# Optimization experiments

Hardware: AMD Instinct MI355X
Metric: run time of the kernel (lower is better)

Reference implementation:

```python
import jax, jax.numpy as jnp
import numpy as np

TOPK = 10
HID = 512
RHID = 150
CH = 32


def _gru(x, Wi, Wh, bi, bh):
    """torch nn.GRU (1 layer, batch_first) with gate order r,z,n. x: [B,T,D]."""
    H = Wh.shape[1]
    xi = x @ Wi.T + bi  # [B,T,3H] precompute input projections

    def step(h, xt):
        gh = h @ Wh.T + bh
        r = jax.nn.sigmoid(xt[:, :H] + gh[:, :H])
        z = jax.nn.sigmoid(xt[:, H:2 * H] + gh[:, H:2 * H])
        n = jnp.tanh(xt[:, 2 * H:] + r * gh[:, 2 * H:])
        h_new = (1.0 - z) * n + z * h
        return h_new, h_new

    h0 = jnp.zeros((x.shape[0], H), x.dtype)
    hT, ys = jax.lax.scan(step, h0, jnp.swapaxes(xi, 0, 1))
    return jnp.swapaxes(ys, 0, 1), hT


def reference(window, emb, w_init, w_root, arma_b, Wi1, Wh1, bi1, bh1,
              Wi2, Wh2, bi2, bh2, W_fc, b_fc):
    B, T, N = window.shape
    # --- SingleEmbedding (post-warmup): cosine similarity + per-row top-k ---
    Wn = emb / jnp.clip(jnp.linalg.norm(emb, axis=1, keepdims=True), 1e-8, None)
    A = Wn @ Wn.T
    A = A * (1.0 - jnp.eye(N, dtype=A.dtype))  # fill_diagonal_(0)
    A = jnp.maximum(A, 0.0)                    # clamp(0)
    vals, idx = jax.lax.top_k(A, TOPK)         # [N, TOPK]
    # zero-valued edges kept with weight 0: identical math (zero degree/message contribution)
    src = jnp.repeat(jnp.arange(N), TOPK)      # edge source = row i
    dst = idx.reshape(-1)                      # edge dest = col j
    attr = vals.reshape(-1)
    # --- batch edges over B (offset b*N), then over T (offset t*B*N), as in torch code ---
    boff = jnp.arange(B) * N
    bsrc = (src[None, :] + boff[:, None]).reshape(-1)   # [B*E]
    bdst = (dst[None, :] + boff[:, None]).reshape(-1)
    battr = jnp.tile(attr, B)
    toff = jnp.arange(T) * (B * N)
    fsrc = (bsrc[None, :] + toff[:, None]).reshape(-1)  # [T*B*E]
    fdst = (bdst[None, :] + toff[:, None]).reshape(-1)
    fattr = jnp.tile(battr, T)
    Ntot = B * N * T
    # node layout (b, n, t): flat row = (b*N + n)*T + t  (faithful to torch view order)
    x = jnp.transpose(window, (0, 2, 1)).reshape(Ntot, 1)
    # --- ARMAConv: 1 stack, 1 layer, GELU, gcn_norm without self-loops ---
    deg = jax.ops.segment_sum(fattr, fdst, num_segments=Ntot)
    dinv = jnp.where(deg > 0, jax.lax.rsqrt(jnp.where(deg > 0, deg, 1.0)), 0.0)
    enorm = dinv[fsrc] * fattr * dinv[fdst]
    h = x @ w_init                                            # [Ntot, CH]
    agg = jax.ops.segment_sum(h[fsrc] * enorm[:, None], fdst, num_segments=Ntot)
    out = jax.nn.gelu(agg + x @ w_root + arma_b, approximate=False)
    # --- add node embedding, GRU encode ---
    xt = out.reshape(B, N, T, CH).transpose(0, 2, 1, 3) + emb  # [B,T,N,CH]
    xt = xt.reshape(B, T, N * CH)
    _, h_end = _gru(xt, Wi1, Wh1, bi1, bh1)                   # [B, HID]
    # --- ReconstructionModel: repeat_interleave(T, dim=1).view(B,T,-1) then GRU+fc ---
    hrep = jnp.repeat(h_end, T, axis=1).reshape(B, T, HID)
    dec, _ = _gru(hrep, Wi2, Wh2, bi2, bh2)                   # [B,T,RHID]
    return dec @ W_fc.T + b_fc


def setup_inputs():
    key = jax.random.key(0)
    ks = jax.random.split(key, 10)
    B, T, N = 32, 100, 150
    d_in = N * CH
    return {
        "window": jax.random.normal(ks[0], (B, T, N), jnp.float32),
        "emb": jax.random.normal(ks[1], (N, CH), jnp.float32) * 0.3,
        "w_init": jax.random.normal(ks[2], (1, CH), jnp.float32) * 0.5,
        "w_root": jax.random.normal(ks[3], (1, CH), jnp.float32) * 0.5,
        "arma_b": jnp.zeros((CH,), jnp.float32),
        "Wi1": jax.random.normal(ks[4], (3 * HID, d_in), jnp.float32) * (1.0 / np.sqrt(d_in)),
        "Wh1": jax.random.normal(ks[5], (3 * HID, HID), jnp.float32) * (1.0 / np.sqrt(HID)),
        "bi1": jnp.zeros((3 * HID,), jnp.float32),
        "bh1": jnp.zeros((3 * HID,), jnp.float32),
        "Wi2": jax.random.normal(ks[6], (3 * RHID, HID), jnp.float32) * (1.0 / np.sqrt(HID)),
        "Wh2": jax.random.normal(ks[7], (3 * RHID, RHID), jnp.float32) * (1.0 / np.sqrt(RHID)),
        "bi2": jnp.zeros((3 * RHID,), jnp.float32),
        "bh2": jnp.zeros((3 * RHID,), jnp.float32),
        "W_fc": jax.random.normal(ks[8], (N, RHID), jnp.float32) * (1.0 / np.sqrt(RHID)),
        "b_fc": jnp.zeros((N,), jnp.float32),
    }
```

## Files before the change

### kernel.cpp

```cpp
#include <hip/hip_runtime.h>
#include <hip/hip_fp16.h>
#include <math.h>

typedef _Float16 f16;
typedef _Float16 half8 __attribute__((ext_vector_type(8)));
typedef _Float16 half4 __attribute__((ext_vector_type(4)));
typedef float float4v __attribute__((ext_vector_type(4)));
typedef float float2v __attribute__((ext_vector_type(2)));
typedef unsigned int uint4v __attribute__((ext_vector_type(4)));

#define AS1 __attribute__((address_space(1)))
#define AS3 __attribute__((address_space(3)))

constexpr size_t alup(size_t x){ return (x + 255) & ~(size_t)255; }
constexpr size_t OFF_MT   = 0;
constexpr size_t OFF_DEG  = alup(OFF_MT + 150*150*4);
constexpr size_t OFF_HT0  = alup(OFF_DEG + 150*4);
constexpr size_t OFF_HT1  = alup(OFF_HT0 + (size_t)32*512*4);
constexpr size_t OFF_WI2P = alup(OFF_HT1 + (size_t)32*512*4);
constexpr size_t OFF_WFCP = alup(OFF_WI2P + (size_t)512*512*2);
constexpr size_t OFF_DECB = alup(OFF_WFCP + (size_t)256*192*2);
constexpr size_t ZONE_END = alup(OFF_DECB + (size_t)3200*192*2);
constexpr size_t OFF_EDST = ZONE_END;
constexpr size_t OFF_EVAL = alup(OFF_EDST + 1500*4);
constexpr size_t OFF_XF   = alup(OFF_EVAL + 1500*4);
constexpr size_t OFF_SS   = alup(OFF_XF + (size_t)480000*4);
constexpr size_t OFF_XT   = alup(OFF_SS + (size_t)480000*4);
constexpr size_t OFF_WI1H = alup(OFF_XT + (size_t)3200*4800*2);
constexpr size_t OFF_XI1  = alup(OFF_WI1H + (size_t)1536*4800*2);
constexpr size_t OFF_U    = alup(OFF_XI1 + (size_t)3200*1536*2);
constexpr size_t OFF_XI2  = alup(OFF_U + (size_t)3200*512*2);

static __device__ __forceinline__ float fsig(float x){ return 1.0f/(1.0f + __expf(-x)); }
static __device__ __forceinline__ float ftanh(float x){
    x = fminf(fmaxf(x, -15.f), 15.f);
    float e = __expf(2.0f*x);
    return (e - 1.0f)/(e + 1.0f);
}

__global__ void k_topk(const float* __restrict__ emb, int* __restrict__ EDST,
                       float* __restrict__ EVAL, float* __restrict__ DEG) {
    __shared__ float WnT[32*152];
    __shared__ float invn[160];
    __shared__ float As[160];
    int tid = threadIdx.x;
    int i = blockIdx.x;
    for (int idx = tid; idx < 4800; idx += 256) {
        int jj = idx >> 5, c = idx & 31;
        WnT[c*152 + jj] = emb[idx];
    }
    __syncthreads();
    if (tid < 150) {
        float s = 0.f;
        #pragma unroll
        for (int c = 0; c < 32; ++c) { float v = WnT[c*152 + tid]; s += v*v; }
        invn[tid] = 1.0f / fmaxf(sqrtf(s), 1e-8f);
    }
    __syncthreads();
    for (int idx = tid; idx < 4800; idx += 256) {
        int jj = idx >> 5, c = idx & 31;
        WnT[c*152 + jj] *= invn[jj];
    }
    __syncthreads();
    int j = tid;
    if (j < 150) {
        float a = 0.f;
        #pragma unroll
        for (int c = 0; c < 32; ++c) a += WnT[c*152 + i] * WnT[c*152 + j];
        a = (j == i) ? 0.f : fmaxf(a, 0.f);
        As[j] = a;
    }
    __syncthreads();
    if (j < 150) {
        float aj = As[j];
        int cnt = 0;
        for (int m = 0; m < 150; ++m) {
            float am = As[m];
            cnt += (am > aj) || (am == aj && m < j);
        }
        if (cnt < 10) {
            EDST[i*10 + cnt] = j;
            EVAL[i*10 + cnt] = aj;
            atomicAdd(&DEG[j], aj);
        }
    }
}

__global__ void k_prep(const int* __restrict__ EDST, const float* __restrict__ EVAL,
                       const float* __restrict__ DEG, float* __restrict__ MT,
                       const float* __restrict__ Wi1, f16* __restrict__ WI1H,
                       const float* __restrict__ Wi2, f16* __restrict__ WI2P,
                       const float* __restrict__ W_fc, f16* __restrict__ WFCP,
                       const float* __restrict__ window, float* __restrict__ XF) {
    int b = blockIdx.x, tid = threadIdx.x;
    if (b == 0) {
        __shared__ float dinv[160];
        if (tid < 150) {
            float d = DEG[tid];
            dinv[tid] = (d > 0.f) ? rsqrtf(d) : 0.f;
        }
        __syncthreads();
        for (int e = tid; e < 1500; e += 256) {
            int src = e / 10;
            int dst = EDST[e];
            MT[src*150 + dst] = dinv[src] * EVAL[e] * dinv[dst];
        }
    } else if (b < 28801) {
        int idx = (b - 1)*256 + tid;
        WI1H[idx] = (f16)Wi1[idx];
    } else if (b < 29701) {
        int idx = (b - 28801)*256 + tid;
        WI2P[idx] = (f16)Wi2[idx];
    } else if (b < 29789) {
        int idx = (b - 29701)*256 + tid;
        if (idx < 22500) {
            int r = idx / 150, c = idx % 150;
            WFCP[r*192 + c] = (f16)W_fc[idx];
        }
    } else {
        int idx = (b - 29789)*256 + tid;
        float v = window[idx];
        int bb = idx / 15000;
        int r = idx % 15000;
        int t = r / 150, n = r % 150;
        XF[bb*15000 + n*100 + t] = v;
    }
}

__global__ void k_conv(const float* __restrict__ XF, const float* __restrict__ MT,
                       float* __restrict__ SS) {
    __shared__ float xs[152];
    int tid = threadIdx.x;
    int base = blockIdx.x * 150;
    if (tid < 150) xs[tid] = XF[base + tid];
    __syncthreads();
    if (tid < 150) {
        float s = 0.f;
        for (int m = 0; m < 150; ++m) s += MT[m*150 + tid] * xs[m];
        SS[base + tid] = s;
    }
}

__global__ void k_xt(const float* __restrict__ SS, const float* __restrict__ XF,
                     const float* __restrict__ w_init, const float* __restrict__ w_root,
                     const float* __restrict__ arma_b, const float* __restrict__ emb,
                     f16* __restrict__ xt) {
    __shared__ float ssl[152];
    __shared__ float xfl[152];
    int tid = threadIdx.x;
    int bid = blockIdx.x;
    int b = bid / 100, t = bid % 100;
    if (tid < 150) {
        int f = b*15000 + tid*100 + t;
        ssl[tid] = SS[f];
        xfl[tid] = XF[f];
    }
    __syncthreads();
    for (int e = tid; e < 4800; e += 256) {
        int n = e >> 5, c = e & 31;
        float pre = ssl[n]*w_init[c] + xfl[n]*w_root[c] + arma_b[c];
        float g = 0.5f * pre * (1.0f + erff(pre * 0.70710678118654752f));
        xt[(size_t)bid*4800 + e] = (f16)(g + emb[e]);
    }
}

template <typename TC>
__global__ void k_gemm(const f16* __restrict__ A, const f16* __restrict__ Bm,
                       const float* __restrict__ bias, TC* __restrict__ C,
                       int K, int ldc, int nvalid, int ntm) {
    __shared__ f16 As[128*64];
    __shared__ f16 Bs[128*64];
    int tid = threadIdx.x;
    int lane = tid & 63, wave = tid >> 6;
    int wm = wave >> 1, wn = wave & 1;
    int tm = blockIdx.x % ntm, tn = blockIdx.x / ntm;
    int m0 = tm * 128, n0 = tn * 128;
    int lrow = lane & 15, quad = lane >> 4;

    float4v acc[4][4];
    #pragma unroll
    for (int mi = 0; mi < 4; ++mi)
        #pragma unroll
        for (int ni = 0; ni < 4; ++ni)
            acc[mi][ni] = (float4v){0.f, 0.f, 0.f, 0.f};

    for (int k0 = 0; k0 < K; k0 += 64) {
        #pragma unroll
        for (int i = 0; i < 4; ++i) {
            int cid = i*256 + tid;
            int row = cid >> 3, cq = cid & 7;
            int cbase = cid & ~63;
            const f16* ga = A + (size_t)(m0+row)*K + k0 + cq*8;
            __builtin_amdgcn_global_load_lds((const AS1 void*)ga, (AS3 void*)(As + cbase*8), 16, 0, 0);
            const f16* gb = Bm + (size_t)(n0+row)*K + k0 + cq*8;
            __builtin_amdgcn_global_load_lds((const AS1 void*)gb, (AS3 void*)(Bs + cbase*8), 16, 0, 0);
        }
        __syncthreads();
        #pragma unroll
        for (int kk = 0; kk < 2; ++kk) {
            half8 aF[4], bF[4];
            #pragma unroll
            for (int mi = 0; mi < 4; ++mi)
                aF[mi] = *(const half8*)&As[(wm*64 + mi*16 + lrow)*64 + kk*32 + quad*8];
            #pragma unroll
            for (int ni = 0; ni < 4; ++ni)
                bF[ni] = *(const half8*)&Bs[(wn*64 + ni*16 + lrow)*64 + kk*32 + quad*8];
            #pragma unroll
            for (int mi = 0; mi < 4; ++mi)
                #pragma unroll
                for (int ni = 0; ni < 4; ++ni)
                    acc[mi][ni] = __builtin_amdgcn_mfma_f32_16x16x32_f16(aF[mi], bF[ni], acc[mi][ni], 0, 0, 0);
        }
        __syncthreads();
    }

    #pragma unroll
    for (int ni = 0; ni < 4; ++ni) {
        int gcol = n0 + wn*64 + ni*16 + lrow;
        if (gcol >= nvalid) continue;
        float bv = bias[gcol];
        #pragma unroll
        for (int mi = 0; mi < 4; ++mi) {
            int growb = m0 + wm*64 + mi*16 + quad*4;
            #pragma unroll
            for (int r = 0; r < 4; ++r)
                C[(size_t)(growb + r)*ldc + gcol] = (TC)(acc[mi][ni][r] + bv);
        }
    }
}

__global__ __launch_bounds__(256, 1)
void k_gru1(const f16* __restrict__ xi1, const float* __restrict__ Wh1,
            const float* __restrict__ bh1, unsigned* __restrict__ ht0,
            unsigned* __restrict__ ht1) {
    __shared__ __align__(16) f16 hA[16*640];
    __shared__ float ghs[192];
    int tid = threadIdx.x;
    int g = blockIdx.x & 15;
    int j = blockIdx.x >> 4;
    int b0 = g * 2;
    int lane = tid & 63, wave = tid >> 6;
    int lrow = lane & 15, quad = lane >> 4;

    half8 Bf0[16], Bf1[16];
    if (wave < 3) {
        #pragma unroll
        for (int tile = 0; tile < 2; ++tile) {
            int rr = (wave*2 + tile)*16 + lrow;
            int grow = (rr >> 5)*512 + (j << 5) + (rr & 31);
            const float* wp = Wh1 + (size_t)grow*512 + quad*8;
            #pragma unroll
            for (int k0 = 0; k0 < 16; ++k0) {
                float4v w0 = *(const float4v*)(wp + k0*32);
                float4v w1 = *(const float4v*)(wp + k0*32 + 4);
                half8 hb;
                hb[0]=(f16)w0[0]; hb[1]=(f16)w0[1]; hb[2]=(f16)w0[2]; hb[3]=(f16)w0[3];
                hb[4]=(f16)w1[0]; hb[5]=(f16)w1[1]; hb[6]=(f16)w1[2]; hb[7]=(f16)w1[3];
                if (tile == 0) Bf0[k0] = hb; else Bf1[k0] = hb;
            }
        }
    }

    float hold = 0.f, bhr = 0.f, bhz = 0.f, bhn = 0.f;
    f16 xir = (f16)0.f, xiz = (f16)0.f, xin = (f16)0.f;
    size_t xb = 0;
    if (tid < 64) {
        int bl = tid >> 5, i = tid & 31;
        int col = (j << 5) + i;
        bhr = bh1[col]; bhz = bh1[512 + col]; bhn = bh1[1024 + col];
        xb = (size_t)((b0 + bl)*100)*1536 + col;
        xir = xi1[xb]; xiz = xi1[xb + 512]; xin = xi1[xb + 1024];
    }
    int sbl = tid >> 7;
    int kb  = (tid & 127) << 2;

    for (int t = 0; t < 100; ++t) {
        const unsigned* cur = (t & 1) ? ht1 : ht0;
        unsigned* nxt = (t & 1) ? ht0 : ht1;
        {
            const unsigned* p = cur + (size_t)(b0 + sbl)*512 + kb;
            uint4v A4;
            unsigned tagw = (unsigned)t << 16;
            for (;;) {
                asm volatile("global_load_dwordx4 %0, %1, off sc0 sc1\n\ts_waitcnt vmcnt(0)"
                             : "=v"(A4) : "v"(p) : "memory");
                if ((A4[0] & 0xffff0000u) == tagw && (A4[1] & 0xffff0000u) == tagw &&
                    (A4[2] & 0xffff0000u) == tagw && (A4[3] & 0xffff0000u) == tagw) break;
                __builtin_amdgcn_s_sleep(1);
            }
            union { unsigned short s[4]; half4 h; } cv;
            cv.s[0] = (unsigned short)A4[0]; cv.s[1] = (unsigned short)A4[1];
            cv.s[2] = (unsigned short)A4[2]; cv.s[3] = (unsigned short)A4[3];
            *(half4*)&hA[(kb >> 5)*640 + sbl*40 + (kb & 31)] = cv.h;
        }
        __syncthreads();

        if (wave < 3) {
            float4v a0a = (float4v){0.f,0.f,0.f,0.f}, a0b = a0a, a1a = a0a, a1b = a0a;
            const f16* aB = &hA[lrow*40 + quad*8];
            #pragma unroll
            for (int k0 = 0; k0 < 16; k0 += 2) {
                half8 a0 = *(const half8*)(aB + k0*640);
                half8 a1 = *(const half8*)(aB + (k0+1)*640);
                a0a = __builtin_amdgcn_mfma_f32_16x16x32_f16(a0, Bf0[k0], a0a, 0, 0, 0);
                a1a = __builtin_amdgcn_mfma_f32_16x16x32_f16(a0, Bf1[k0], a1a, 0, 0, 0);
                a0b = __builtin_amdgcn_mfma_f32_16x16x32_f16(a1, Bf0[k0+1], a0b, 0, 0, 0);
                a1b = __builtin_amdgcn_mfma_f32_16x16x32_f16(a1, Bf1[k0+1], a1b, 0, 0, 0);
            }
            if (lane < 16) {
                int n0 = wave*2, n1 = n0 + 1;
                ghs[n0*16 + lane]      = a0a[0] + a0b[0];
                ghs[96 + n0*16 + lane] = a0a[1] + a0b[1];
                ghs[n1*16 + lane]      = a1a[0] + a1b[0];
                ghs[96 + n1*16 + lane] = a1a[1] + a1b[1];
            }
        }
        __syncthreads();

        if (tid < 64) {
            int bl = tid >> 5, i = tid & 31;
            float xr_ = (float)xir, xz_ = (float)xiz, xn_ = (float)xin;
            int tn = (t < 99) ? t + 1 : 99;
            size_t xo = xb + (size_t)tn*1536;
            xir = xi1[xo]; xiz = xi1[xo + 512]; xin = xi1[xo + 1024];
            float gr = ghs[bl*96 + i]      + bhr;
            float gz = ghs[bl*96 + 32 + i] + bhz;
            float gn = ghs[bl*96 + 64 + i] + bhn;
            float r = fsig(xr_ + gr);
            float z = fsig(xz_ + gz);
            float n = ftanh(xn_ + r*gn);
            float hnew = (1.f - z)*n + z*hold;
            hold = hnew;
            union { f16 h; unsigned short s; } hb; hb.h = (f16)hnew;
            unsigned pk = ((unsigned)(t + 1) << 16) | (unsigned)hb.s;
            __hip_atomic_store(nxt + (size_t)(b0 + bl)*512 + (j << 5) + i, pk,
                               __ATOMIC_RELAXED, __HIP_MEMORY_SCOPE_AGENT);
        }
    }
}

__global__ void k_build_u(const unsigned* __restrict__ ht0, f16* __restrict__ u) {
    int idx = blockIdx.x * blockDim.x + threadIdx.x;
    if (idx >= 32*100*512) return;
    int b = idx / 51200;
    int r = idx % 51200;
    int t = r >> 9, k = r & 511;
    union { unsigned short s; f16 h; } cv;
    cv.s = (unsigned short)ht0[(b << 9) + ((t*512 + k) / 100)];
    u[idx] = cv.h;
}

__global__ __launch_bounds__(512, 2)
void k_gru2(const f16* __restrict__ xi2, const float* __restrict__ Wh2,
            const float* __restrict__ bh2, f16* __restrict__ decb) {
    __shared__ float hs2[152];
    __shared__ float ghs2[456];
    __shared__ float xis2[456];
    int tid = threadIdx.x;
    int b = blockIdx.x;
    bool act = tid < 450;
    float2v w[75];
    float bhv = 0.f;
    if (act) {
        const float2v* wrow = (const float2v*)&Wh2[tid*150];
        #pragma unroll
        for (int k = 0; k < 75; ++k) w[k] = wrow[k];
        bhv = bh2[tid];
    }
    if (tid < 152) hs2[tid] = 0.f;
    size_t row0 = (size_t)b * 100 * 512;
    float xr = act ? (float)xi2[row0 + tid] : 0.f;
    __syncthreads();

    for (int t = 0; t < 100; ++t) {
        if (act) xis2[tid] = xr;
        __syncthreads();
        if (act) {
            float a = bhv;
            #pragma unroll
            for (int k = 0; k < 75; ++k)
                a += w[k][0] * hs2[2*k] + w[k][1] * hs2[2*k+1];
            ghs2[tid] = a;
        }
        int tn = (t < 99) ? t + 1 : 99;
        if (act) xr = (float)xi2[((size_t)b*100 + tn)*512 + tid];
        __syncthreads();
        if (tid < 150) {
            int i = tid;
            float r = fsig(xis2[i] + ghs2[i]);
            float z = fsig(xis2[150 + i] + ghs2[150 + i]);
            float n = ftanh(xis2[300 + i] + r * ghs2[300 + i]);
            float hnew = (1.f - z) * n + z * hs2[i];
            hs2[i] = hnew;
            decb[((size_t)b*100 + t)*192 + i] = (f16)hnew;
        }
        __syncthreads();
    }
}

extern "C" void kernel_launch(void* const* d_in, const int* in_sizes, int n_in,
                              void* d_out, int out_size, void* d_ws, size_t ws_size,
                              hipStream_t stream) {
    const float* window = (const float*)d_in[0];
    const float* emb    = (const float*)d_in[1];
    const float* w_init = (const float*)d_in[2];
    const float* w_root = (const float*)d_in[3];
    const float* arma_b = (const float*)d_in[4];
    const float* Wi1    = (const float*)d_in[5];
    const float* Wh1    = (const float*)d_in[6];
    const float* bi1    = (const float*)d_in[7];
    const float* bh1    = (const float*)d_in[8];
    const float* Wi2    = (const float*)d_in[9];
    const float* Wh2    = (const float*)d_in[10];
    const float* bi2    = (const float*)d_in[11];
    const float* bh2    = (const float*)d_in[12];
    const float* W_fc   = (const float*)d_in[13];
    const float* b_fc   = (const float*)d_in[14];
    float* out = (float*)d_out;

    char* ws = (char*)d_ws;
    float*    MT   = (float*)(ws + OFF_MT);
    float*    DEG  = (float*)(ws + OFF_DEG);
    unsigned* HT0  = (unsigned*)(ws + OFF_HT0);
    unsigned* HT1  = (unsigned*)(ws + OFF_HT1);
    f16*      WI2P = (f16*)  (ws + OFF_WI2P);
    f16*      WFCP = (f16*)  (ws + OFF_WFCP);
    f16*      DECB = (f16*)  (ws + OFF_DECB);
    int*      EDST = (int*)  (ws + OFF_EDST);
    float*    EVAL = (float*)(ws + OFF_EVAL);
    float*    XF   = (float*)(ws + OFF_XF);
    float*    SS   = (float*)(ws + OFF_SS);
    f16*      XT   = (f16*)  (ws + OFF_XT);
    f16*      WI1H = (f16*)  (ws + OFF_WI1H);
    f16*      XI1H = (f16*)  (ws + OFF_XI1);
    f16*      UB   = (f16*)  (ws + OFF_U);
    f16*      XI2H = (f16*)  (ws + OFF_XI2);

    hipMemsetAsync(d_ws, 0, ZONE_END, stream);

    k_topk<<<150, 256, 0, stream>>>(emb, EDST, EVAL, DEG);

    k_prep<<<31664, 256, 0, stream>>>(EDST, EVAL, DEG, MT,
                                      Wi1, WI1H, Wi2, WI2P, W_fc, WFCP, window, XF);

    k_conv<<<3200, 256, 0, stream>>>(XF, MT, SS);
    k_xt<<<3200, 256, 0, stream>>>(SS, XF, w_init, w_root, arma_b, emb, XT);

    k_gemm<f16><<<25*12, 256, 0, stream>>>(XT, WI1H, bi1, XI1H, 4800, 1536, 1536, 25);

    k_gru1<<<256, 256, 0, stream>>>(XI1H, Wh1, bh1, HT0, HT1);

    k_build_u<<<(32*100*512 + 255)/256, 256, 0, stream>>>(HT0, UB);

    k_gemm<f16><<<25*4, 256, 0, stream>>>(UB, WI2P, bi2, XI2H, 512, 512, 450, 25);

    k_gru2<<<32, 512, 0, stream>>>(XI2H, Wh2, bh2, DECB);

    k_gemm<float><<<25*2, 256, 0, stream>>>(DECB, WFCP, b_fc, out, 192, 150, 150, 25);

    (void)in_sizes; (void)n_in; (void)out_size; (void)ws_size;
}
```

Before: 615.0 us.

## Use MFMA for GRU2 recurrent matvec with fp16 padded Wh2 held in registers

```diff
diff --git a/kernel.cpp b/kernel.cpp
--- a/kernel.cpp
+++ b/kernel.cpp
@@ -19,7 +19,8 @@
 constexpr size_t OFF_HT1  = alup(OFF_HT0 + (size_t)32*512*4);
 constexpr size_t OFF_WI2P = alup(OFF_HT1 + (size_t)32*512*4);
 constexpr size_t OFF_WFCP = alup(OFF_WI2P + (size_t)512*512*2);
-constexpr size_t OFF_DECB = alup(OFF_WFCP + (size_t)256*192*2);
+constexpr size_t OFF_WH2P = alup(OFF_WFCP + (size_t)256*192*2);
+constexpr size_t OFF_DECB = alup(OFF_WH2P + (size_t)512*160*2);
 constexpr size_t ZONE_END = alup(OFF_DECB + (size_t)3200*192*2);
 constexpr size_t OFF_EDST = ZONE_END;
 constexpr size_t OFF_EVAL = alup(OFF_EDST + 1500*4);
@@ -91,6 +92,7 @@
                        const float* __restrict__ Wi1, f16* __restrict__ WI1H,
                        const float* __restrict__ Wi2, f16* __restrict__ WI2P,
                        const float* __restrict__ W_fc, f16* __restrict__ WFCP,
+                       const float* __restrict__ Wh2, f16* __restrict__ WH2P,
                        const float* __restrict__ window, float* __restrict__ XF) {
     int b = blockIdx.x, tid = threadIdx.x;
     if (b == 0) {
@@ -117,8 +119,14 @@
             int r = idx / 150, c = idx % 150;
             WFCP[r*192 + c] = (f16)W_fc[idx];
         }
+    } else if (b < 30053) {
+        int idx = (b - 29789)*256 + tid;
+        if (idx < 67500) {
+            int r = idx / 150, c = idx % 150;
+            WH2P[r*160 + c] = (f16)Wh2[idx];
+        }
     } else {
-        int idx = (b - 29789)*256 + tid;
+        int idx = (b - 30053)*256 + tid;
         float v = window[idx];
         int bb = idx / 15000;
         int r = idx % 15000;
@@ -350,49 +358,67 @@
     u[idx] = cv.h;
 }
 
-__global__ __launch_bounds__(512, 2)
-void k_gru2(const f16* __restrict__ xi2, const float* __restrict__ Wh2,
+__global__ __launch_bounds__(256, 1)
+void k_gru2(const f16* __restrict__ xi2, const f16* __restrict__ wh2p,
             const float* __restrict__ bh2, f16* __restrict__ decb) {
-    __shared__ float hs2[152];
-    __shared__ float ghs2[456];
-    __shared__ float xis2[456];
+    __shared__ __align__(16) f16 hA[5*640];
+    __shared__ float ghs[512];
     int tid = threadIdx.x;
     int b = blockIdx.x;
-    bool act = tid < 450;
-    float2v w[75];
-    float bhv = 0.f;
-    if (act) {
-        const float2v* wrow = (const float2v*)&Wh2[tid*150];
-        #pragma unroll
-        for (int k = 0; k < 75; ++k) w[k] = wrow[k];
-        bhv = bh2[tid];
-    }
-    if (tid < 152) hs2[tid] = 0.f;
-    size_t row0 = (size_t)b * 100 * 512;
-    float xr = act ? (float)xi2[row0 + tid] : 0.f;
+    int lane = tid & 63, wave = tid >> 6;
+    int lrow = lane & 15, quad = lane >> 4;
+
+    for (int i = tid; i < 5*640; i += 256) hA[i] = (f16)0.f;
+
+    half8 Bf[8][5];
+    #pragma unroll
+    for (int tt = 0; tt < 8; ++tt) {
+        int rn = (wave*8 + tt)*16 + lrow;
+        const f16* wp = wh2p + (size_t)rn*160 + quad*8;
+        #pragma unroll
+        for (int k0 = 0; k0 < 5; ++k0)
+            Bf[tt][k0] = *(const half8*)(wp + k0*32);
+    }
+
+    float hold = 0.f, bhr = 0.f, bhz = 0.f, bhn = 0.f;
+    f16 xr = (f16)0.f, xz = (f16)0.f, xn = (f16)0.f;
+    size_t xbase = (size_t)b * 100 * 512;
+    if (tid < 150) {
+        bhr = bh2[tid]; bhz = bh2[150 + tid]; bhn = bh2[300 + tid];
+        xr = xi2[xbase + tid]; xz = xi2[xbase + 150 + tid]; xn = xi2[xbase + 300 + tid];
+    }
     __syncthreads();
 
     for (int t = 0; t < 100; ++t) {
-        if (act) xis2[tid] = xr;
-        __syncthreads();
-        if (act) {
-            float a = bhv;
-            #pragma unroll
-            for (int k = 0; k < 75; ++k)
-                a += w[k][0] * hs2[2*k] + w[k][1] * hs2[2*k+1];
-            ghs2[tid] = a;
-        }
-        int tn = (t < 99) ? t + 1 : 99;
-        if (act) xr = (float)xi2[((size_t)b*100 + tn)*512 + tid];
-        __syncthreads();
+        float4v acc[8];
+        #pragma unroll
+        for (int tt = 0; tt < 8; ++tt) acc[tt] = (float4v){0.f,0.f,0.f,0.f};
+        #pragma unroll
+        for (int k0 = 0; k0 < 5; ++k0) {
+            half8 a = *(const half8*)&hA[k0*640 + lrow*40 + quad*8];
+            #pragma unroll
+            for (int tt = 0; tt < 8; ++tt)
+                acc[tt] = __builtin_amdgcn_mfma_f32_16x16x32_f16(a, Bf[tt][k0], acc[tt], 0, 0, 0);
+        }
+        if (lane < 16) {
+            #pragma unroll
+            for (int tt = 0; tt < 8; ++tt)
+                ghs[(wave*8 + tt)*16 + lane] = acc[tt][0];
+        }
+        __syncthreads();
+
         if (tid < 150) {
-            int i = tid;
-            float r = fsig(xis2[i] + ghs2[i]);
-            float z = fsig(xis2[150 + i] + ghs2[150 + i]);
-            float n = ftanh(xis2[300 + i] + r * ghs2[300 + i]);
-            float hnew = (1.f - z) * n + z * hs2[i];
-            hs2[i] = hnew;
-            decb[((size_t)b*100 + t)*192 + i] = (f16)hnew;
+            float r = fsig((float)xr + ghs[tid] + bhr);
+            float z = fsig((float)xz + ghs[150 + tid] + bhz);
+            float n = ftanh((float)xn + r*(ghs[300 + tid] + bhn));
+            float hnew = (1.f - z)*n + z*hold;
+            hold = hnew;
+            f16 hh = (f16)hnew;
+            hA[(tid >> 5)*640 + (tid & 31)] = hh;
+            decb[((size_t)b*100 + t)*192 + tid] = hh;
+            int tn = (t < 99) ? t + 1 : 99;
+            size_t xo = xbase + (size_t)tn*512;
+            xr = xi2[xo + tid]; xz = xi2[xo + 150 + tid]; xn = xi2[xo + 300 + tid];
         }
         __syncthreads();
     }
@@ -425,6 +451,7 @@
     unsigned* HT1  = (unsigned*)(ws + OFF_HT1);
     f16*      WI2P = (f16*)  (ws + OFF_WI2P);
     f16*      WFCP = (f16*)  (ws + OFF_WFCP);
+    f16*      WH2P = (f16*)  (ws + OFF_WH2P);
     f16*      DECB = (f16*)  (ws + OFF_DECB);
     int*      EDST = (int*)  (ws + OFF_EDST);
     float*    EVAL = (float*)(ws + OFF_EVAL);
@@ -440,8 +467,9 @@
 
     k_topk<<<150, 256, 0, stream>>>(emb, EDST, EVAL, DEG);
 
-    k_prep<<<31664, 256, 0, stream>>>(EDST, EVAL, DEG, MT,
-                                      Wi1, WI1H, Wi2, WI2P, W_fc, WFCP, window, XF);
+    k_prep<<<31928, 256, 0, stream>>>(EDST, EVAL, DEG, MT,
+                                      Wi1, WI1H, Wi2, WI2P, W_fc, WFCP,
+                                      Wh2, WH2P, window, XF);
 
     k_conv<<<3200, 256, 0, stream>>>(XF, MT, SS);
     k_xt<<<3200, 256, 0, stream>>>(SS, XF, w_init, w_root, arma_b, emb, XT);
@@ -454,7 +482,7 @@
 
     k_gemm<f16><<<25*4, 256, 0, stream>>>(UB, WI2P, bi2, XI2H, 512, 512, 450, 25);
 
-    k_gru2<<<32, 512, 0, stream>>>(XI2H, Wh2, bh2, DECB);
+    k_gru2<<<32, 256, 0, stream>>>(XI2H, WH2P, bh2, DECB);
 
     k_gemm<float><<<25*2, 256, 0, stream>>>(DECB, WFCP, b_fc, out, 192, 150, 150, 25);
 
```

Result: faster. 544.1 us (-11.5%).
